# Kernel tuning notes

Hardware: AMD Instinct MI355X
Metric: run time of the kernel (lower is better)

## Reference

```python
import jax, jax.numpy as jnp
import numpy as np

H = 8        # n_attention_heads
D = 512      # model_dimension (full per-head dim in this module!)
DFF = 2048   # feed_forward_internal_dimension
B, T = 8, 1024
EPS = 1e-5


def _layernorm(x, g, b, eps=EPS):
    mu = jnp.mean(x, axis=-1, keepdims=True)
    var = jnp.mean(jnp.square(x - mu), axis=-1, keepdims=True)
    return (x - mu) * jax.lax.rsqrt(var + eps) * g + b


def setup_inputs() -> dict:
    key = jax.random.key(0)
    ks = jax.random.split(key, 16)
    s_d = 1.0 / np.sqrt(D)
    s_c = 1.0 / np.sqrt(H * D)
    s_f = 1.0 / np.sqrt(DFF)
    return {
        "x":   jax.random.normal(ks[0], (B, T, D), jnp.float32),
        # per-head projections, stored (in, out); stacked over heads
        "Wq":  jax.random.normal(ks[1], (H, D, D), jnp.float32) * s_d,
        "bq":  jax.random.normal(ks[2], (H, D), jnp.float32) * 0.02,
        "Wk":  jax.random.normal(ks[3], (H, D, D), jnp.float32) * s_d,
        "bk":  jax.random.normal(ks[4], (H, D), jnp.float32) * 0.02,
        "Wv":  jax.random.normal(ks[5], (H, D, D), jnp.float32) * s_d,
        "bv":  jax.random.normal(ks[6], (H, D), jnp.float32) * 0.02,
        "Wo":  jax.random.normal(ks[7], (H * D, D), jnp.float32) * s_c,
        "bo":  jax.random.normal(ks[8], (D,), jnp.float32) * 0.02,
        "ln1_g": 1.0 + 0.1 * jax.random.normal(ks[9], (D,), jnp.float32),
        "ln1_b": 0.1 * jax.random.normal(ks[10], (D,), jnp.float32),
        "W1":  jax.random.normal(ks[11], (D, DFF), jnp.float32) * s_d,
        "b1":  jax.random.normal(ks[12], (DFF,), jnp.float32) * 0.02,
        "W2":  jax.random.normal(ks[13], (DFF, D), jnp.float32) * s_f,
        "b2":  jax.random.normal(ks[14], (D,), jnp.float32) * 0.02,
        "ln2_g": 1.0 + 0.1 * jax.random.normal(ks[15], (D,), jnp.float32),
        "ln2_b": jnp.zeros((D,), jnp.float32),
    }


def reference(x, Wq, bq, Wk, bk, Wv, bv, Wo, bo, ln1_g, ln1_b,
              W1, b1, W2, b2, ln2_g, ln2_b):
    # --- multi-head attention (each head uses the FULL d_model) ---
    # q,k,v: [H, B, T, D]
    q = jnp.einsum("btd,hde->hbte", x, Wq) + bq[:, None, None, :]
    k = jnp.einsum("btd,hde->hbte", x, Wk) + bk[:, None, None, :]
    v = jnp.einsum("btd,hde->hbte", x, Wv) + bv[:, None, None, :]
    scores = jnp.einsum("hbte,hbse->hbts", q, k) * (D ** -0.5)  # [H,B,T,T]
    attn = jax.nn.softmax(scores, axis=-1)
    heads = jnp.einsum("hbts,hbse->hbte", attn, v)  # [H,B,T,D]
    # concat heads along features: [B,T,H*D]
    concat = jnp.transpose(heads, (1, 2, 0, 3)).reshape(x.shape[0], x.shape[1], -1)
    mha = concat @ Wo + bo
    # residual + LayerNorm (dropout_p = 0)
    y1 = _layernorm(mha + x, ln1_g, ln1_b)
    # --- FFN: note source applies ReLU AFTER the second Linear, then skip ---
    ff = jax.nn.relu((y1 @ W1 + b1) @ W2 + b2) + y1
    out = _layernorm(ff, ln2_g, ln2_b)
    return out
```

## Files before the change

kernel.cpp:

```cpp
#include <hip/hip_runtime.h>

using u16 = unsigned short;
using bf16x8 = __attribute__((ext_vector_type(8))) short;
using f32x4 = __attribute__((ext_vector_type(4))) float;
using f32x16 = __attribute__((ext_vector_type(16))) float;

__device__ __forceinline__ u16 f2bf(float f) {
  unsigned x = __float_as_uint(f);
  x += 0x7fffu + ((x >> 16) & 1u);
  return (u16)(x >> 16);
}

__device__ __forceinline__ void gl2lds16(const u16* g, u16* l) {
  __builtin_amdgcn_global_load_lds(
      (const __attribute__((address_space(1))) unsigned int*)g,
      (__attribute__((address_space(3))) unsigned int*)l, 16, 0, 0);
}

__global__ __launch_bounds__(256) void cvt_all(
    const float* __restrict__ x, u16* __restrict__ Krep, u16* __restrict__ XT,
    const float* __restrict__ Wq, const float* __restrict__ Wk,
    const float* __restrict__ Wv, const float* __restrict__ Wo,
    const float* __restrict__ W1, const float* __restrict__ W2,
    u16* __restrict__ Wqb, u16* __restrict__ Wkb, u16* __restrict__ Wvb,
    u16* __restrict__ WoT, u16* __restrict__ W1T, u16* __restrict__ W2T)
{
  int b = blockIdx.x, tid = threadIdx.x;
  if (b < 10240) {
    const float* s; u16* d; int i;
    if (b < 4096)      { s = x;  d = Krep; i = b * 1024 + tid * 4; }
    else if (b < 6144) { s = Wq; d = Wqb;  i = (b - 4096) * 1024 + tid * 4; }
    else if (b < 8192) { s = Wk; d = Wkb;  i = (b - 6144) * 1024 + tid * 4; }
    else               { s = Wv; d = Wvb;  i = (b - 8192) * 1024 + tid * 4; }
    float4 v = *(const float4*)(s + i);
    ushort4 o;
    o.x = f2bf(v.x); o.y = f2bf(v.y); o.z = f2bf(v.z); o.w = f2bf(v.w);
    *(ushort4*)(d + i) = o;
    return;
  }
  __shared__ float T[32][33];
  const float* s; u16* d; int K, N, k0, n0;
  int i = b - 10240;
  if (i < 4096) {
    int b8 = i >> 9, j = i & 511;
    s = x + (size_t)b8 * 524288; d = XT + (size_t)b8 * 524288;
    K = 1024; N = 512; n0 = (j % 16) * 32; k0 = (j / 16) * 32;
  } else if (i < 6144) {
    int j = i - 4096;
    s = Wo; d = WoT; K = 4096; N = 512; n0 = (j % 16) * 32; k0 = (j / 16) * 32;
  } else if (i < 7168) {
    int j = i - 6144;
    s = W1; d = W1T; K = 512; N = 2048; n0 = (j % 64) * 32; k0 = (j / 64) * 32;
  } else {
    int j = i - 7168;
    s = W2; d = W2T; K = 2048; N = 512; n0 = (j % 16) * 32; k0 = (j / 16) * 32;
  }
  int r = tid >> 3, c4 = (tid & 7) << 2;
  float4 v = *(const float4*)(s + (size_t)(k0 + r) * N + n0 + c4);
  T[r][c4 + 0] = v.x; T[r][c4 + 1] = v.y; T[r][c4 + 2] = v.z; T[r][c4 + 3] = v.w;
  __syncthreads();
  ushort4 o;
  o.x = f2bf(T[c4 + 0][r]); o.y = f2bf(T[c4 + 1][r]);
  o.z = f2bf(T[c4 + 2][r]); o.w = f2bf(T[c4 + 3][r]);
  *(ushort4*)(d + (size_t)(n0 + r) * K + k0 + c4) = o;
}

__global__ __launch_bounds__(256) void wk_bias(
    const float* __restrict__ Wk, const float* __restrict__ bq,
    float* __restrict__ wbuf)
{
  int r = blockIdx.x * 4 + (threadIdx.x >> 6);
  int lane = threadIdx.x & 63;
  int h = r >> 9, a = r & 511;
  const float* row = Wk + ((size_t)h * 512 + a) * 512 + lane * 8;
  const float* bqp = bq + h * 512 + lane * 8;
  float4 w0 = *(const float4*)row, w1 = *(const float4*)(row + 4);
  float4 b0 = *(const float4*)bqp, b1 = *(const float4*)(bqp + 4);
  float s = w0.x * b0.x + w0.y * b0.y + w0.z * b0.z + w0.w * b0.w +
            w1.x * b1.x + w1.y * b1.y + w1.z * b1.z + w1.w * b1.w;
  #pragma unroll
  for (int off = 1; off < 64; off <<= 1) s += __shfl_xor(s, off);
  if (lane == 0) wbuf[r] = s;
}

__global__ __launch_bounds__(256) void bo_fold(
    const float* __restrict__ bv, const float* __restrict__ Wo,
    const float* __restrict__ bo, float* __restrict__ bop)
{
  __shared__ float part[16][17];
  int ei = threadIdx.x & 15, ch = threadIdx.x >> 4;
  int e = blockIdx.x * 16 + ei;
  float s = 0.f;
  for (int k = ch * 256; k < ch * 256 + 256; k++)
    s += bv[k] * Wo[(size_t)k * 512 + e];
  part[ei][ch] = s;
  __syncthreads();
  if (threadIdx.x < 16) {
    float t = bo[blockIdx.x * 16 + threadIdx.x];
    #pragma unroll
    for (int c = 0; c < 16; c++) t += part[threadIdx.x][c];
    bop[blockIdx.x * 16 + threadIdx.x] = t;
  }
}

template<int BM>
__global__ __launch_bounds__(256) void gemm_bt(
    const u16* __restrict__ A, const u16* __restrict__ Bt,
    const float* __restrict__ bias, void* __restrict__ Cout,
    int M, int N, int K, int lda, int ldb, long long kzoff,
    long long sBz, long long sbz, long long sCzBytes, int out_mode)
{
  constexpr int MT = BM / 32;
  constexpr int TILE = BM * 32 + 128 * 32;
  __shared__ __align__(16) u16 smem[2 * TILE];
  const f32x4 zero4 = {0.f, 0.f, 0.f, 0.f};

  const u16* Ap = A + (size_t)blockIdx.z * (size_t)kzoff;
  const u16* Bp = Bt + (size_t)blockIdx.z * (size_t)(sBz + kzoff);
  const float* biasp = bias ? bias + (size_t)blockIdx.z * sbz : nullptr;
  char* Cp = (char*)Cout + (size_t)blockIdx.z * sCzBytes;

  int P = gridDim.x * gridDim.y;
  int p = blockIdx.x + gridDim.x * blockIdx.y;
  int f = (p & 7) * (P >> 3) + (p >> 3);
  int bx = f % gridDim.x, by = f / gridDim.x;

  int tid = threadIdx.x;
  int lane = tid & 63, wave = tid >> 6;
  int m = lane & 15, quad = lane >> 4;
  int wm = (wave >> 1) * (BM / 2), wn = (wave & 1) * 64;
  int m0 = by * BM, n0 = bx * 128;
  int lr = lane >> 2, lc = (lane & 3) << 3;

  auto stage = [&](int buf, int k0) {
    u16* As = smem + buf * TILE;
    u16* Bs = As + BM * 32;
    #pragma unroll
    for (int i = 0; i < BM / 64; i++) {
      int rb = i * 64 + wave * 16;
      gl2lds16(Ap + (size_t)(m0 + rb + lr) * lda + k0 + lc, &As[rb * 32]);
    }
    #pragma unroll
    for (int i = 0; i < 2; i++) {
      int rb = i * 64 + wave * 16;
      gl2lds16(Bp + (size_t)(n0 + rb + lr) * ldb + k0 + lc, &Bs[rb * 32]);
    }
  };

  f32x4 acc[MT][4];
  #pragma unroll
  for (int i = 0; i < MT; i++)
    #pragma unroll
    for (int j = 0; j < 4; j++) acc[i][j] = zero4;

  stage(0, 0);
  asm volatile("s_waitcnt vmcnt(0)" ::: "memory");
  __builtin_amdgcn_s_barrier();

  int nt = K >> 5;
  int cur = 0;
  for (int t = 0; t < nt; t++) {
    if (t + 1 < nt) stage(cur ^ 1, (t + 1) << 5);

    u16* As = smem + cur * TILE;
    u16* Bs = As + BM * 32;
    bf16x8 af[MT], bfr[4];
    #pragma unroll
    for (int tt = 0; tt < MT; tt++)
      af[tt] = *(const bf16x8*)&As[(wm + tt * 16 + m) * 32 + quad * 8];
    #pragma unroll
    for (int tt = 0; tt < 4; tt++)
      bfr[tt] = *(const bf16x8*)&Bs[(wn + tt * 16 + m) * 32 + quad * 8];
    #pragma unroll
    for (int mt = 0; mt < MT; mt++)
      #pragma unroll
      for (int nt2 = 0; nt2 < 4; nt2++)
        acc[mt][nt2] = __builtin_amdgcn_mfma_f32_16x16x32_bf16(af[mt], bfr[nt2],
                                                               acc[mt][nt2], 0, 0, 0);
    asm volatile("s_waitcnt vmcnt(0)" ::: "memory");
    __builtin_amdgcn_s_barrier();
    cur ^= 1;
  }

  if (out_mode == 2) {
    u16* Ts = smem;
    int b2 = m0 >> 10, t20 = m0 & 1023;
    int half = wave >> 1;
    #pragma unroll
    for (int mt = 0; mt < MT; mt++) {
      #pragma unroll
      for (int nt2 = 0; nt2 < 4; nt2++) {
        int colc = wn + nt2 * 16 + m;
        float bb = biasp ? biasp[n0 + colc] : 0.f;
        #pragma unroll
        for (int r = 0; r < 4; r++)
          Ts[colc * 40 + half * 16 + quad * 4 + r] = f2bf(acc[mt][nt2][r] + bb);
      }
      __syncthreads();
      #pragma unroll
      for (int it = 0; it < 2; it++) {
        int c = (tid >> 2) + 64 * it;
        int j = tid & 3;
        bf16x8 v = *(const bf16x8*)&Ts[c * 40 + j * 8];
        int tg = t20 + (j >> 1) * (BM / 2) + mt * 16 + (j & 1) * 8;
        *(bf16x8*)((u16*)Cp + ((size_t)b2 * 512 + n0 + c) * 1024 + tg) = v;
      }
      __syncthreads();
    }
    return;
  }

  #pragma unroll
  for (int nt2 = 0; nt2 < 4; nt2++) {
    int col = n0 + wn + nt2 * 16 + m;
    float bb = biasp ? biasp[col] : 0.f;
    #pragma unroll
    for (int mt = 0; mt < MT; mt++) {
      #pragma unroll
      for (int r = 0; r < 4; r++) {
        int row = m0 + wm + mt * 16 + quad * 4 + r;
        float v = acc[mt][nt2][r] + bb;
        if (out_mode == 1) {
          ((u16*)Cp)[(size_t)row * N + col] = f2bf(v);
        } else {
          ((float*)Cp)[(size_t)row * N + col] = v;
        }
      }
    }
  }
}

__global__ __launch_bounds__(256) void gemm_t8(
    const u16* __restrict__ A, const u16* __restrict__ Mt,
    const float* __restrict__ wbuf, u16* __restrict__ Tg)
{
  constexpr int TILE = 8192;
  __shared__ __align__(16) u16 smem[2 * TILE];
  const f32x4 zero4 = {0.f, 0.f, 0.f, 0.f};

  int h = blockIdx.z;
  const u16* Bp = Mt + (size_t)h * 262144;
  const float* biasp = wbuf + h * 512;
  u16* Og = Tg + (size_t)h * 4194304;

  int P = gridDim.x * gridDim.y;
  int p = blockIdx.x + gridDim.x * blockIdx.y;
  int f = (p & 7) * (P >> 3) + (p >> 3);
  int bx = f % gridDim.x, by = f / gridDim.x;

  int tid = threadIdx.x;
  int lane = tid & 63, wave = tid >> 6;
  int m = lane & 15, quad = lane >> 4;
  int wm = (wave >> 1) * 64, wn = (wave & 1) * 64;
  int m0 = by * 128, n0 = bx * 128;
  int lr = lane >> 2, lc = (lane & 3) << 3;

  auto stage = [&](int buf, int k0) {
    u16* As = smem + buf * TILE;
    u16* Bs = As + 4096;
    #pragma unroll
    for (int i = 0; i < 2; i++) {
      int rb = i * 64 + wave * 16;
      gl2lds16(A + (size_t)(m0 + rb + lr) * 512 + k0 + lc, &As[rb * 32]);
      gl2lds16(Bp + (size_t)(n0 + rb + lr) * 512 + k0 + lc, &Bs[rb * 32]);
    }
  };

  f32x4 acc[4][4];
  #pragma unroll
  for (int i = 0; i < 4; i++)
    #pragma unroll
    for (int j = 0; j < 4; j++) acc[i][j] = zero4;

  stage(0, 0);
  asm volatile("s_waitcnt vmcnt(0)" ::: "memory");
  __builtin_amdgcn_s_barrier();

  int cur = 0;
  for (int t = 0; t < 16; t++) {
    if (t + 1 < 16) stage(cur ^ 1, (t + 1) << 5);

    u16* As = smem + cur * TILE;
    u16* Bs = As + 4096;
    bf16x8 af[4], bfr[4];
    #pragma unroll
    for (int tt = 0; tt < 4; tt++) {
      af[tt]  = *(const bf16x8*)&As[(wm + tt * 16 + m) * 32 + quad * 8];
      bfr[tt] = *(const bf16x8*)&Bs[(wn + tt * 16 + m) * 32 + quad * 8];
    }
    #pragma unroll
    for (int mt = 0; mt < 4; mt++)
      #pragma unroll
      for (int nt = 0; nt < 4; nt++)
        acc[mt][nt] = __builtin_amdgcn_mfma_f32_16x16x32_bf16(af[mt], bfr[nt],
                                                              acc[mt][nt], 0, 0, 0);
    asm volatile("s_waitcnt vmcnt(0)" ::: "memory");
    __builtin_amdgcn_s_barrier();
    cur ^= 1;
  }

  #pragma unroll
  for (int nt = 0; nt < 4; nt++) {
    int col = n0 + wn + nt * 16 + m;
    float bb = biasp[col];
    #pragma unroll
    for (int mt = 0; mt < 4; mt++) {
      #pragma unroll
      for (int r = 0; r < 4; r++) {
        int row = m0 + wm + mt * 16 + quad * 4 + r;
        Og[(size_t)row * 512 + col] = f2bf(acc[mt][nt][r] + bb);
      }
    }
  }
}

__global__ __launch_bounds__(256, 2) void attn_kernel(
    const u16* __restrict__ Tg, const u16* __restrict__ Krep,
    const u16* __restrict__ XT, u16* __restrict__ Oc, int h0)
{
  __shared__ __align__(16) u16 Kt[32][520];
  __shared__ __align__(16) u16 Vt[512 * 32];
  __shared__ __align__(16) u16 Pl[64][40];
  __shared__ float lred[64];
  const f32x4 zero4 = {0.f, 0.f, 0.f, 0.f};
  const f32x16 zero16 = {0.f,0.f,0.f,0.f,0.f,0.f,0.f,0.f,
                         0.f,0.f,0.f,0.f,0.f,0.f,0.f,0.f};

  int b = blockIdx.x, qb = blockIdx.y, z = blockIdx.z;
  int h = h0 + z;

  size_t hb = ((size_t)z * 8 + b) * (size_t)(1024 * 512);
  const u16* Tp = Tg + hb;
  const u16* Kp = Krep + (size_t)b * (size_t)(1024 * 512);
  const u16* Vp = XT + (size_t)b * (size_t)(512 * 1024);

  int tid = threadIdx.x, lane = tid & 63, wave = tid >> 6;
  int m = lane & 15, quad = lane >> 4;
  int l31 = lane & 31, hi = lane >> 5;
  int qh = wave >> 1, dh = wave & 1;
  int q0 = qb * 64 + wave * 16;

  int vr = lane >> 2;
  int vc = (((lane & 3) ^ ((lane >> 3) & 3)) << 3);
  int vswz = (l31 >> 1) & 3;

  bf16x8 aq[16];
  #pragma unroll
  for (int kc = 0; kc < 16; kc++)
    aq[kc] = *(const bf16x8*)(Tp + (size_t)(q0 + m) * 512 + kc * 32 + quad * 8);

  f32x16 o[8];
  #pragma unroll
  for (int dt = 0; dt < 8; dt++) o[dt] = zero16;
  float lsum_acc[4] = {0.f, 0.f, 0.f, 0.f};
  const float scale = 0.04419417382415922f;

  #pragma unroll
  for (int r = 0; r < 8; r++) {
    int row = wave * 8 + r;
    gl2lds16(Kp + (size_t)row * 512 + lane * 8, &Kt[row][0]);
  }
  #pragma unroll
  for (int j = 0; j < 8; j++) {
    int rb = wave * 128 + j * 16;
    gl2lds16(Vp + (size_t)(rb + vr) * 1024 + vc, &Vt[rb * 32]);
  }

  for (int kt = 0; kt < 32; kt++) {
    asm volatile("s_waitcnt vmcnt(8)" ::: "memory");
    __builtin_amdgcn_sched_barrier(0);
    __builtin_amdgcn_s_barrier();
    __builtin_amdgcn_sched_barrier(0);

    f32x4 s0 = zero4, s1 = zero4;
    #pragma unroll
    for (int kc = 0; kc < 16; kc++) {
      bf16x8 bk0 = *(const bf16x8*)&Kt[m][kc * 32 + quad * 8];
      bf16x8 bk1 = *(const bf16x8*)&Kt[m + 16][kc * 32 + quad * 8];
      s0 = __builtin_amdgcn_mfma_f32_16x16x32_bf16(aq[kc], bk0, s0, 0, 0, 0);
      s1 = __builtin_amdgcn_mfma_f32_16x16x32_bf16(aq[kc], bk1, s1, 0, 0, 0);
    }

    #pragma unroll
    for (int r = 0; r < 4; r++) {
      float e0 = __expf(s0[r] * scale);
      float e1 = __expf(s1[r] * scale);
      u16 p0 = f2bf(e0), p1 = f2bf(e1);
      int prow = wave * 16 + quad * 4 + r;
      Pl[prow][m] = p0;
      Pl[prow][m + 16] = p1;
      lsum_acc[r] += __uint_as_float((unsigned)p0 << 16) +
                     __uint_as_float((unsigned)p1 << 16);
    }

    asm volatile("s_waitcnt vmcnt(0) lgkmcnt(0)" ::: "memory");
    __builtin_amdgcn_sched_barrier(0);
    __builtin_amdgcn_s_barrier();
    __builtin_amdgcn_sched_barrier(0);

    if (kt < 31) {
      int kr1 = (kt + 1) * 32;
      #pragma unroll
      for (int r = 0; r < 8; r++) {
        int row = wave * 8 + r;
        gl2lds16(Kp + (size_t)(kr1 + row) * 512 + lane * 8, &Kt[row][0]);
      }
    }

    const u16* PlRow = &Pl[qh * 32 + l31][0];
    #pragma unroll
    for (int ks = 0; ks < 2; ks++) {
      bf16x8 pa = *(const bf16x8*)(PlRow + ks * 16 + hi * 8);
      #pragma unroll
      for (int dt = 0; dt < 8; dt++) {
        int rr = dh * 256 + dt * 32 + l31;
        int cc2 = (((ks * 2 + hi) ^ vswz) << 3);
        bf16x8 bv = *(const bf16x8*)&Vt[rr * 32 + cc2];
        o[dt] = __builtin_amdgcn_mfma_f32_32x32x16_bf16(pa, bv, o[dt], 0, 0, 0);
      }
    }

    asm volatile("s_waitcnt lgkmcnt(0)" ::: "memory");
    __builtin_amdgcn_sched_barrier(0);
    __builtin_amdgcn_s_barrier();
    __builtin_amdgcn_sched_barrier(0);

    if (kt < 31) {
      int kr1 = (kt + 1) * 32;
      #pragma unroll
      for (int j = 0; j < 8; j++) {
        int rb = wave * 128 + j * 16;
        gl2lds16(Vp + (size_t)(rb + vr) * 1024 + kr1 + vc, &Vt[rb * 32]);
      }
    }
  }

  #pragma unroll
  for (int r = 0; r < 4; r++) {
    float t = lsum_acc[r];
    t += __shfl_xor(t, 1); t += __shfl_xor(t, 2);
    t += __shfl_xor(t, 4); t += __shfl_xor(t, 8);
    lsum_acc[r] = t;
  }
  if (m == 0) {
    #pragma unroll
    for (int r = 0; r < 4; r++)
      lred[wave * 16 + quad * 4 + r] = lsum_acc[r];
  }
  __syncthreads();

  float linv[16];
  #pragma unroll
  for (int g = 0; g < 4; g++) {
    float4 t = *(const float4*)&lred[qh * 32 + 8 * g + 4 * hi];
    linv[4 * g + 0] = 1.f / t.x; linv[4 * g + 1] = 1.f / t.y;
    linv[4 * g + 2] = 1.f / t.z; linv[4 * g + 3] = 1.f / t.w;
  }

  size_t obase = (size_t)b * 1024 + qb * 64 + qh * 32;
  #pragma unroll
  for (int dt = 0; dt < 8; dt++) {
    int dcol = dh * 256 + dt * 32 + l31;
    #pragma unroll
    for (int reg = 0; reg < 16; reg++) {
      int rowq = (reg & 3) + 8 * (reg >> 2) + 4 * hi;
      Oc[((obase + rowq) * 8 + h) * 512 + dcol] = f2bf(o[dt][reg] * linv[reg]);
    }
  }
}

__global__ __launch_bounds__(256) void ln_kernel(
    const float* __restrict__ xin0, const float* __restrict__ xin1,
    const float* __restrict__ bias, const float* __restrict__ res,
    const float* __restrict__ gam, const float* __restrict__ bet,
    float* __restrict__ outf, u16* __restrict__ outb, int do_relu)
{
  __shared__ float red[4];
  __shared__ float red2[4];
  int row = blockIdx.x, t = threadIdx.x;
  size_t base = (size_t)row * 512;
  float a0 = xin0[base + t] + bias[t];
  float a1 = xin0[base + 256 + t] + bias[256 + t];
  if (xin1) { a0 += xin1[base + t]; a1 += xin1[base + 256 + t]; }
  if (do_relu) { a0 = fmaxf(a0, 0.f); a1 = fmaxf(a1, 0.f); }
  a0 += res[base + t]; a1 += res[base + 256 + t];

  float s = a0 + a1;
  #pragma unroll
  for (int off = 32; off > 0; off >>= 1) s += __shfl_xor(s, off);
  if ((t & 63) == 0) red[t >> 6] = s;
  __syncthreads();
  float mu = (red[0] + red[1] + red[2] + red[3]) * (1.f / 512.f);

  float d0 = a0 - mu, d1 = a1 - mu;
  float q = d0 * d0 + d1 * d1;
  #pragma unroll
  for (int off = 32; off > 0; off >>= 1) q += __shfl_xor(q, off);
  if ((t & 63) == 0) red2[t >> 6] = q;
  __syncthreads();
  float var = (red2[0] + red2[1] + red2[2] + red2[3]) * (1.f / 512.f);
  float rs = rsqrtf(var + 1e-5f);

  float o0 = d0 * rs * gam[t] + bet[t];
  float o1 = d1 * rs * gam[t + 256] + bet[t + 256];
  outf[base + t] = o0;
  outf[base + 256 + t] = o1;
  if (outb) { outb[base + t] = f2bf(o0); outb[base + 256 + t] = f2bf(o1); }
}

extern "C" void kernel_launch(void* const* d_in, const int* in_sizes, int n_in,
                              void* d_out, int out_size, void* d_ws, size_t ws_size,
                              hipStream_t stream) {
  const float* x   = (const float*)d_in[0];
  const float* Wq  = (const float*)d_in[1];
  const float* bq  = (const float*)d_in[2];
  const float* Wk  = (const float*)d_in[3];
  const float* bk  = (const float*)d_in[4];
  const float* Wv  = (const float*)d_in[5];
  const float* bv  = (const float*)d_in[6];
  const float* Wo  = (const float*)d_in[7];
  const float* bo  = (const float*)d_in[8];
  const float* g1  = (const float*)d_in[9];
  const float* bn1 = (const float*)d_in[10];
  const float* W1  = (const float*)d_in[11];
  const float* bf1 = (const float*)d_in[12];
  const float* W2  = (const float*)d_in[13];
  const float* bf2 = (const float*)d_in[14];
  const float* g2  = (const float*)d_in[15];
  const float* bn2 = (const float*)d_in[16];
  (void)bk;

  char* ws = (char*)d_ws;
  u16* Krep = (u16*)(ws + 0);
  u16* xb   = Krep;
  u16* Wqb = (u16*)(ws + 67108864);
  u16* Wkb = (u16*)(ws + 71303168);
  u16* Wvb = (u16*)(ws + 75497472);
  u16* WoT = (u16*)(ws + 79691776);
  u16* W1T = (u16*)(ws + 83886080);
  u16* W2T = (u16*)(ws + 85983232);
  u16* Mt  = (u16*)(ws + 88080384);
  float* wbuf = (float*)(ws + 92274688);
  u16* cc  = (u16*)(ws + 92291072);
  u16* Tg  = (u16*)(ws + 159399936);
  u16* XT  = (u16*)(ws + 226508800);
  u16* WvWoT = (u16*)(ws + 234897408);
  float* bop = (float*)(ws + 239091712);
  float* y1f  = (float*)(ws + 159399936);
  u16*   y1b  = (u16*)(ws + 176177152);
  float* mha0 = (float*)(ws + 184565760);
  float* mha1 = (float*)(ws + 201342976);
  u16*   ff1  = (u16*)(ws + 92291072);
  float* ff20 = (float*)(ws + 125845504);
  float* ff21 = (float*)(ws + 142622720);

  bo_fold<<<32, 256, 0, stream>>>(bv, Wo, bo, bop);
  cvt_all<<<18432, 256, 0, stream>>>(x, Krep, XT, Wq, Wk, Wv, Wo, W1, W2,
                                     Wqb, Wkb, Wvb, WoT, W1T, W2T);
  gemm_bt<128><<<dim3(4, 4, 8), 256, 0, stream>>>(Wkb, Wqb, nullptr, Mt,
      512, 512, 512, 512, 512, 262144LL, 0LL, 0LL, 524288LL, 1);
  wk_bias<<<1024, 256, 0, stream>>>(Wk, bq, wbuf);
  gemm_bt<128><<<dim3(4, 4, 8), 256, 0, stream>>>(WoT, Wvb, nullptr, WvWoT,
      512, 4096, 512, 4096, 512, 512LL, 261632LL, 0LL, 1024LL, 1);

  gemm_t8<<<dim3(4, 64, 8), 256, 0, stream>>>(xb, Mt, wbuf, Tg);
  attn_kernel<<<dim3(8, 16, 8), 256, 0, stream>>>(Tg, Krep, XT, cc, 0);

  gemm_bt<64><<<dim3(4, 128, 2), 256, 0, stream>>>(cc, WvWoT, nullptr, mha0,
      8192, 512, 2048, 4096, 4096, 2048LL, 0LL, 0LL, 16777216LL, 0);
  ln_kernel<<<8192, 256, 0, stream>>>(mha0, mha1, bop, x, g1, bn1, y1f, y1b, 0);

  gemm_bt<128><<<dim3(16, 64, 1), 256, 0, stream>>>(y1b, W1T, bf1, ff1,
      8192, 2048, 512, 512, 512, 0LL, 0LL, 0LL, 0LL, 1);

  gemm_bt<64><<<dim3(4, 128, 2), 256, 0, stream>>>(ff1, W2T, nullptr, ff20,
      8192, 512, 1024, 2048, 2048, 1024LL, 0LL, 0LL, 16777216LL, 0);

  ln_kernel<<<8192, 256, 0, stream>>>(ff20, ff21, bf2, y1f, g2, bn2,
                                      (float*)d_out, nullptr, 1);
}
```

Before: 555.5 us.

## Fold W1·W2 into one FFN weight since no activation sits between them

```diff
diff --git a/kernel.cpp b/kernel.cpp
--- a/kernel.cpp
+++ b/kernel.cpp
@@ -23,15 +23,16 @@
     const float* __restrict__ Wv, const float* __restrict__ Wo,
     const float* __restrict__ W1, const float* __restrict__ W2,
     u16* __restrict__ Wqb, u16* __restrict__ Wkb, u16* __restrict__ Wvb,
-    u16* __restrict__ WoT, u16* __restrict__ W1T, u16* __restrict__ W2T)
+    u16* __restrict__ WoT, u16* __restrict__ W1b, u16* __restrict__ W2T)
 {
   int b = blockIdx.x, tid = threadIdx.x;
-  if (b < 10240) {
+  if (b < 11264) {
     const float* s; u16* d; int i;
-    if (b < 4096)      { s = x;  d = Krep; i = b * 1024 + tid * 4; }
-    else if (b < 6144) { s = Wq; d = Wqb;  i = (b - 4096) * 1024 + tid * 4; }
-    else if (b < 8192) { s = Wk; d = Wkb;  i = (b - 6144) * 1024 + tid * 4; }
-    else               { s = Wv; d = Wvb;  i = (b - 8192) * 1024 + tid * 4; }
+    if (b < 4096)       { s = x;  d = Krep; i = b * 1024 + tid * 4; }
+    else if (b < 6144)  { s = Wq; d = Wqb;  i = (b - 4096) * 1024 + tid * 4; }
+    else if (b < 8192)  { s = Wk; d = Wkb;  i = (b - 6144) * 1024 + tid * 4; }
+    else if (b < 10240) { s = Wv; d = Wvb;  i = (b - 8192) * 1024 + tid * 4; }
+    else                { s = W1; d = W1b;  i = (b - 10240) * 1024 + tid * 4; }
     float4 v = *(const float4*)(s + i);
     ushort4 o;
     o.x = f2bf(v.x); o.y = f2bf(v.y); o.z = f2bf(v.z); o.w = f2bf(v.w);
@@ -40,7 +41,7 @@
   }
   __shared__ float T[32][33];
   const float* s; u16* d; int K, N, k0, n0;
-  int i = b - 10240;
+  int i = b - 11264;
   if (i < 4096) {
     int b8 = i >> 9, j = i & 511;
     s = x + (size_t)b8 * 524288; d = XT + (size_t)b8 * 524288;
@@ -48,11 +49,8 @@
   } else if (i < 6144) {
     int j = i - 4096;
     s = Wo; d = WoT; K = 4096; N = 512; n0 = (j % 16) * 32; k0 = (j / 16) * 32;
-  } else if (i < 7168) {
+  } else {
     int j = i - 6144;
-    s = W1; d = W1T; K = 512; N = 2048; n0 = (j % 64) * 32; k0 = (j / 64) * 32;
-  } else {
-    int j = i - 7168;
     s = W2; d = W2T; K = 2048; N = 512; n0 = (j % 16) * 32; k0 = (j / 16) * 32;
   }
   int r = tid >> 3, c4 = (tid & 7) << 2;
@@ -83,23 +81,23 @@
   if (lane == 0) wbuf[r] = s;
 }
 
-__global__ __launch_bounds__(256) void bo_fold(
-    const float* __restrict__ bv, const float* __restrict__ Wo,
-    const float* __restrict__ bo, float* __restrict__ bop)
+__global__ __launch_bounds__(256) void vec_fold(
+    const float* __restrict__ v, const float* __restrict__ W,
+    const float* __restrict__ c, float* __restrict__ out, int kc)
 {
   __shared__ float part[16][17];
   int ei = threadIdx.x & 15, ch = threadIdx.x >> 4;
   int e = blockIdx.x * 16 + ei;
   float s = 0.f;
-  for (int k = ch * 256; k < ch * 256 + 256; k++)
-    s += bv[k] * Wo[(size_t)k * 512 + e];
+  for (int k = ch * kc; k < ch * kc + kc; k++)
+    s += v[k] * W[(size_t)k * 512 + e];
   part[ei][ch] = s;
   __syncthreads();
   if (threadIdx.x < 16) {
-    float t = bo[blockIdx.x * 16 + threadIdx.x];
-    #pragma unroll
-    for (int c = 0; c < 16; c++) t += part[threadIdx.x][c];
-    bop[blockIdx.x * 16 + threadIdx.x] = t;
+    float t = c[blockIdx.x * 16 + threadIdx.x];
+    #pragma unroll
+    for (int cc = 0; cc < 16; cc++) t += part[threadIdx.x][cc];
+    out[blockIdx.x * 16 + threadIdx.x] = t;
   }
 }
 
@@ -534,10 +532,12 @@
   u16* Krep = (u16*)(ws + 0);
   u16* xb   = Krep;
   u16* Wqb = (u16*)(ws + 67108864);
+  u16* WcT  = (u16*)(ws + 67108864);
   u16* Wkb = (u16*)(ws + 71303168);
+  float* bcp = (float*)(ws + 71303168);
   u16* Wvb = (u16*)(ws + 75497472);
   u16* WoT = (u16*)(ws + 79691776);
-  u16* W1T = (u16*)(ws + 83886080);
+  u16* W1b = (u16*)(ws + 83886080);
   u16* W2T = (u16*)(ws + 85983232);
   u16* Mt  = (u16*)(ws + 88080384);
   float* wbuf = (float*)(ws + 92274688);
@@ -550,18 +550,19 @@
   u16*   y1b  = (u16*)(ws + 176177152);
   float* mha0 = (float*)(ws + 184565760);
   float* mha1 = (float*)(ws + 201342976);
-  u16*   ff1  = (u16*)(ws + 92291072);
   float* ff20 = (float*)(ws + 125845504);
-  float* ff21 = (float*)(ws + 142622720);
-
-  bo_fold<<<32, 256, 0, stream>>>(bv, Wo, bo, bop);
+
+  vec_fold<<<32, 256, 0, stream>>>(bv, Wo, bo, bop, 256);
   cvt_all<<<18432, 256, 0, stream>>>(x, Krep, XT, Wq, Wk, Wv, Wo, W1, W2,
-                                     Wqb, Wkb, Wvb, WoT, W1T, W2T);
+                                     Wqb, Wkb, Wvb, WoT, W1b, W2T);
   gemm_bt<128><<<dim3(4, 4, 8), 256, 0, stream>>>(Wkb, Wqb, nullptr, Mt,
       512, 512, 512, 512, 512, 262144LL, 0LL, 0LL, 524288LL, 1);
   wk_bias<<<1024, 256, 0, stream>>>(Wk, bq, wbuf);
+  vec_fold<<<32, 256, 0, stream>>>(bf1, W2, bf2, bcp, 128);
   gemm_bt<128><<<dim3(4, 4, 8), 256, 0, stream>>>(WoT, Wvb, nullptr, WvWoT,
       512, 4096, 512, 4096, 512, 512LL, 261632LL, 0LL, 1024LL, 1);
+  gemm_bt<128><<<dim3(4, 4, 1), 256, 0, stream>>>(W2T, W1b, nullptr, WcT,
+      512, 512, 2048, 2048, 2048, 0LL, 0LL, 0LL, 0LL, 1);
 
   gemm_t8<<<dim3(4, 64, 8), 256, 0, stream>>>(xb, Mt, wbuf, Tg);
   attn_kernel<<<dim3(8, 16, 8), 256, 0, stream>>>(Tg, Krep, XT, cc, 0);
@@ -570,12 +571,9 @@
       8192, 512, 2048, 4096, 4096, 2048LL, 0LL, 0LL, 16777216LL, 0);
   ln_kernel<<<8192, 256, 0, stream>>>(mha0, mha1, bop, x, g1, bn1, y1f, y1b, 0);
 
-  gemm_bt<128><<<dim3(16, 64, 1), 256, 0, stream>>>(y1b, W1T, bf1, ff1,
-      8192, 2048, 512, 512, 512, 0LL, 0LL, 0LL, 0LL, 1);
-
-  gemm_bt<64><<<dim3(4, 128, 2), 256, 0, stream>>>(ff1, W2T, nullptr, ff20,
-      8192, 512, 1024, 2048, 2048, 1024LL, 0LL, 0LL, 16777216LL, 0);
-
-  ln_kernel<<<8192, 256, 0, stream>>>(ff20, ff21, bf2, y1f, g2, bn2,
+  gemm_bt<128><<<dim3(4, 64, 1), 256, 0, stream>>>(y1b, WcT, nullptr, ff20,
+      8192, 512, 512, 512, 512, 0LL, 0LL, 0LL, 0LL, 0);
+
+  ln_kernel<<<8192, 256, 0, stream>>>(ff20, nullptr, bcp, y1f, g2, bn2,
                                       (float*)d_out, nullptr, 1);
 }
```

Result: slower. 632.3 us (+13.8%).
